# Kernel optimization log

Measured on AMD Instinct MI355X. Metric: run time of the kernel, lower is better.

## Reference

```python
import jax, jax.numpy as jnp
import numpy as np

H1, H2, H3 = 128, 64, 32   # hidden sizes from source constants
NT = 2                      # n_targets (P_I_meas, Q_I_meas)
NF = 16                     # n_features
B, T, S = 4096, 200, 20     # batch, history length, OUTPUT_STEPS


def setup_inputs() -> dict:
    key = jax.random.key(0)
    ks = jax.random.split(key, 16)
    s1 = 1.0 / np.sqrt(H1)  # pytorch LSTM init scale
    s2 = 1.0 / np.sqrt(H2)
    s3 = 1.0 / np.sqrt(H3)
    f32 = jnp.float32
    return {
        "x_history": jax.random.normal(ks[0], (B, T, NF), dtype=f32),
        "x_future_refs": jax.random.normal(ks[1], (B, S, NF - NT), dtype=f32),
        "Wih1": jax.random.normal(ks[2], (4 * H1, NF), dtype=f32) * s1,
        "Whh1": jax.random.normal(ks[3], (4 * H1, H1), dtype=f32) * s1,
        "bih1": jax.random.normal(ks[4], (4 * H1,), dtype=f32) * s1,
        "bhh1": jax.random.normal(ks[5], (4 * H1,), dtype=f32) * s1,
        "Wih2": jax.random.normal(ks[6], (4 * H2, H1), dtype=f32) * s2,
        "Whh2": jax.random.normal(ks[7], (4 * H2, H2), dtype=f32) * s2,
        "bih2": jax.random.normal(ks[8], (4 * H2,), dtype=f32) * s2,
        "bhh2": jax.random.normal(ks[9], (4 * H2,), dtype=f32) * s2,
        "Wd": jax.random.normal(ks[10], (H3, H2), dtype=f32) * s2,
        "bd": jax.random.normal(ks[11], (H3,), dtype=f32) * s2,
        "Wf": jax.random.normal(ks[12], (NT, H3), dtype=f32) * s3,
        "bf": jax.random.normal(ks[13], (NT,), dtype=f32) * s3,
        "out_bias": jnp.zeros((NT,), dtype=f32),
    }


def lstm_cell(x, h, c, Wih, Whh, bih, bhh):
    # PyTorch gate order: i, f, g, o
    g = x @ Wih.T + h @ Whh.T + (bih + bhh)
    i, f, gg, o = jnp.split(g, 4, axis=-1)
    c_new = jax.nn.sigmoid(f) * c + jax.nn.sigmoid(i) * jnp.tanh(gg)
    h_new = jax.nn.sigmoid(o) * jnp.tanh(c_new)
    return h_new, c_new


def reference(x_history, x_future_refs, Wih1, Whh1, bih1, bhh1,
              Wih2, Whh2, bih2, bhh2, Wd, bd, Wf, bf, out_bias):
    b = x_history.shape[0]
    dt = x_history.dtype
    h1 = jnp.zeros((b, H1), dt); c1 = jnp.zeros((b, H1), dt)
    h2 = jnp.zeros((b, H2), dt); c2 = jnp.zeros((b, H2), dt)

    # --- encode history: stacked 2-layer LSTM over T steps ---
    def enc_step(carry, xt):
        h1, c1, h2, c2 = carry
        h1, c1 = lstm_cell(xt, h1, c1, Wih1, Whh1, bih1, bhh1)
        h2, c2 = lstm_cell(h1, h2, c2, Wih2, Whh2, bih2, bhh2)
        return (h1, c1, h2, c2), None

    (h1, c1, h2, c2), _ = jax.lax.scan(
        enc_step, (h1, c1, h2, c2), jnp.swapaxes(x_history, 0, 1))

    # last history targets: x_history[:, -1, n_non_targets:]
    cur = x_history[:, -1, NF - NT:]

    def dec_step(carry, ref):
        h1, c1, h2, c2, cur = carry
        xin = jnp.concatenate([ref, cur], axis=1)  # [B, NF]
        h1, c1 = lstm_cell(xin, h1, c1, Wih1, Whh1, bih1, bhh1)
        h2, c2 = lstm_cell(h1, h2, c2, Wih2, Whh2, bih2, bhh2)
        d = jax.nn.relu(h2 @ Wd.T + bd)
        pred = d @ Wf.T + bf + out_bias
        return (h1, c1, h2, c2, pred), pred

    _, preds = jax.lax.scan(
        dec_step, (h1, c1, h2, c2, cur), jnp.swapaxes(x_future_refs, 0, 1))
    return jnp.swapaxes(preds, 0, 1)  # [B, S, NT]
```

## Files before the change

kernel.cpp:

```cpp
#include <hip/hip_runtime.h>

typedef unsigned short u16;
typedef unsigned int u32;

using short8 = __attribute__((ext_vector_type(8))) short;
using f32x4  = __attribute__((ext_vector_type(4))) float;
using float4v = __attribute__((ext_vector_type(4))) float;

#define LOG2E 1.44269504088896340736f

#define X1S 136
#define H2S 72
#define DBS 40
#define XCS 328

__device__ __forceinline__ u16 f2bf(float f) {
  u32 u = __float_as_uint(f);
  return (u16)((u + 0x7FFFu + ((u >> 16) & 1u)) >> 16);
}
__device__ __forceinline__ float sigm(float x) {
  return __builtin_amdgcn_rcpf(1.0f + __builtin_amdgcn_exp2f(-LOG2E * x));
}
__device__ __forceinline__ float tanh_(float x) {
  return 1.0f - 2.0f * __builtin_amdgcn_rcpf(1.0f + __builtin_amdgcn_exp2f(2.0f * LOG2E * x));
}
__device__ __forceinline__ f32x4 mfma_(short8 a, short8 b, f32x4 c) {
  return __builtin_amdgcn_mfma_f32_16x16x32_bf16(a, b, c, 0, 0, 0);
}

__global__ __launch_bounds__(512, 1) void spc_lstm(
    const float* __restrict__ xh,   const float* __restrict__ xfr,
    const float* __restrict__ Wih1, const float* __restrict__ Whh1,
    const float* __restrict__ bih1, const float* __restrict__ bhh1,
    const float* __restrict__ Wih2, const float* __restrict__ Whh2,
    const float* __restrict__ bih2, const float* __restrict__ bhh2,
    const float* __restrict__ Wd,   const float* __restrict__ bd,
    const float* __restrict__ Wf,   const float* __restrict__ bfv,
    const float* __restrict__ ob,   float* __restrict__ out)
{
  __shared__ __align__(16) u16 X1[2][16 * X1S];
  __shared__ __align__(16) u16 H2B[2][16 * H2S];
  __shared__ __align__(16) u16 DB[16 * DBS];
  __shared__ __align__(16) u16 W1xF[32 * 512];
  __shared__ __align__(16) u16 W2F[64 * 512];
  __shared__ __align__(16) u16 WdF[4 * 512];
  __shared__ __align__(16) u16 WfF[512];
  __shared__ __align__(16) u16 XCH[2][16 * XCS];

  const int tid = threadIdx.x;
  const int wv  = tid >> 6;
  const int l   = tid & 63;
  const int c   = l & 15;
  const int q   = l >> 4;
  const int bb  = blockIdx.x << 4;
  const bool isA = (wv < 4);

  short8 w1h[4][4];
  short8 w2h[4][2];
  float  b1r[4];
  float  b2r[4] = {0.f, 0.f, 0.f, 0.f};

  for (int i = tid; i < 2 * 16 * X1S; i += 512) ((u16*)X1)[i] = 0;
  for (int i = tid; i < 2 * 16 * H2S; i += 512) ((u16*)H2B)[i] = 0;
  for (int i = tid; i < 16 * DBS; i += 512) DB[i] = 0;
  for (int i = tid; i < 2 * 16 * XCS; i += 512) ((u16*)XCH)[i] = 0;
  __syncthreads();

  for (int i = tid; i < 64 * 512; i += 512) {
    const int rid = i >> 9, e = i & 511, k = e >> 4, n = e & 15;
    const int ww = rid >> 4, ty = (rid >> 2) & 3, kc = rid & 3;
    const int g = ty * 64 + ww * 16 + n;
    W2F[rid * 512 + ((k >> 3) * 16 + n) * 8 + (k & 7)] = f2bf(Wih2[g * 128 + kc * 32 + k]);
  }
  for (int i = tid; i < 32 * 512; i += 512) {
    const int T = i >> 9, e = i & 511, k = e >> 4, n = e & 15;
    const int ty = T >> 3, uv = T & 7;
    const int g = ty * 128 + uv * 16 + n;
    W1xF[T * 512 + ((k >> 3) * 16 + n) * 8 + (k & 7)] =
        (k < 16) ? f2bf(Wih1[g * 16 + k]) : (u16)0;
  }
  for (int i = tid; i < 4 * 512; i += 512) {
    const int tix = i >> 9, e = i & 511, k = e >> 4, n = e & 15;
    const int ww = tix >> 1, kc2 = tix & 1;
    WdF[tix * 512 + ((k >> 3) * 16 + n) * 8 + (k & 7)] =
        f2bf(Wd[(ww * 16 + n) * 64 + kc2 * 32 + k]);
  }
  {
    const int k = tid >> 4, n = tid & 15;
    if (tid < 512)
      WfF[((k >> 3) * 16 + n) * 8 + (k & 7)] = (n < 2) ? f2bf(Wf[n * 32 + k]) : (u16)0;
  }

  if (!isA) {
    const int i0 = tid - 256;
    #pragma unroll
    for (int p = 0; p < 2; p++) {
      const int idx = i0 + p * 256;
      const int r = idx >> 5, rem = idx & 31, st = rem >> 2, hf = rem & 3;
      const float4v v = *(const float4v*)&xh[(bb + r) * 3200 + st * 16 + hf * 4];
      u16* d = &XCH[0][r * XCS + st * 40 + hf * 4];
      d[0] = f2bf(v[0]); d[1] = f2bf(v[1]); d[2] = f2bf(v[2]); d[3] = f2bf(v[3]);
    }
  }

  #pragma unroll
  for (int ty = 0; ty < 4; ty++) {
    const int g = ty * 128 + wv * 16 + c;
    b1r[ty] = bih1[g] + bhh1[g];
    #pragma unroll
    for (int kc = 0; kc < 4; kc++) {
      short8 v;
      #pragma unroll
      for (int j = 0; j < 8; j++)
        v[j] = (short)f2bf(Whh1[g * 128 + kc * 32 + q * 8 + j]);
      w1h[ty][kc] = v;
    }
  }
  if (isA) {
    #pragma unroll
    for (int ty = 0; ty < 4; ty++) {
      const int g2 = ty * 64 + wv * 16 + c;
      b2r[ty] = bih2[g2] + bhh2[g2];
      #pragma unroll
      for (int kc = 0; kc < 2; kc++) {
        short8 v;
        #pragma unroll
        for (int j = 0; j < 8; j++)
          v[j] = (short)f2bf(Whh2[g2 * 64 + kc * 32 + q * 8 + j]);
        w2h[ty][kc] = v;
      }
    }
  }
  const float bdr = (wv == 4 || wv == 5) ? bd[(wv - 4) * 16 + c] : 0.f;
  const float bfr = (wv == 4 && c < 2) ? (bfv[c] + ob[c]) : 0.f;

  f32x4 c1 = (f32x4){0,0,0,0};
  f32x4 c2 = (f32x4){0,0,0,0};
  __syncthreads();

  for (int t = 0; t <= 220; t++) {
    u16* Xc    = X1[t & 1];
    u16* Xn    = X1[(t + 1) & 1];
    u16* Hprev = H2B[t & 1];
    u16* Hdst  = H2B[(t + 1) & 1];
    const bool dec  = (t >= 201);
    const bool doL1 = (t <= 219);
    const bool doL2 = isA && (t >= 1);

    if (!isA && (t & 7) == 0) {
      const int cm = (t >> 3) + 1;
      if (cm <= 27) {
        u16* dst = XCH[cm & 1];
        const int t0 = cm << 3;
        if (cm <= 24) {
          const int i0 = tid - 256;
          #pragma unroll
          for (int p = 0; p < 2; p++) {
            const int idx = i0 + p * 256;
            const int r = idx >> 5, rem = idx & 31, st = rem >> 2, hf = rem & 3;
            const float4v v = *(const float4v*)&xh[(bb + r) * 3200 + (t0 + st) * 16 + hf * 4];
            u16* d = &dst[r * XCS + st * 40 + hf * 4];
            d[0] = f2bf(v[0]); d[1] = f2bf(v[1]); d[2] = f2bf(v[2]); d[3] = f2bf(v[3]);
          }
        } else {
          for (int e = tid - 256; e < 16 * 8 * 14; e += 256) {
            const int r = e / 112, rem2 = e % 112, st = rem2 / 14, f = rem2 % 14;
            const int s8 = t0 + st;
            if (s8 < 220)
              dst[r * XCS + st * 40 + f] = f2bf(xfr[(bb + r) * 280 + (s8 - 200) * 14 + f]);
          }
          if (cm == 25) {
            const int e = tid - 256;
            if (e < 32) {
              const int r = e >> 1, f = 14 + (e & 1);
              dst[r * XCS + f] = f2bf(xh[(bb + r) * 3200 + 199 * 16 + f]);
            }
          }
        }
      }
    }

    if (doL2) {
      f32x4 acc2[4];
      #pragma unroll
      for (int ty = 0; ty < 4; ty++)
        acc2[ty] = (f32x4){b2r[ty], b2r[ty], b2r[ty], b2r[ty]};
      #pragma unroll
      for (int kc = 0; kc < 4; kc++) {
        const short8 fhi = *(const short8*)&Xc[c * X1S + kc * 32 + q * 8];
        #pragma unroll
        for (int ty = 0; ty < 4; ty++) {
          const short8 wf_ = *(const short8*)&W2F[(wv * 16 + ty * 4 + kc) * 512 + l * 8];
          acc2[ty] = mfma_(fhi, wf_, acc2[ty]);
        }
      }
      #pragma unroll
      for (int kc = 0; kc < 2; kc++) {
        const short8 hhi = *(const short8*)&Hprev[c * H2S + kc * 32 + q * 8];
        #pragma unroll
        for (int ty = 0; ty < 4; ty++)
          acc2[ty] = mfma_(hhi, w2h[ty][kc], acc2[ty]);
      }
      const int u = wv * 16 + c;
      #pragma unroll
      for (int r = 0; r < 4; r++) {
        float ig = sigm(acc2[0][r]);
        float fg = sigm(acc2[1][r]);
        float gg = tanh_(acc2[2][r]);
        float og = sigm(acc2[3][r]);
        float cn = fg * c2[r] + ig * gg;
        float hn = og * tanh_(cn);
        c2[r] = cn;
        Hdst[(q * 4 + r) * H2S + u] = f2bf(hn);
      }
    }

    if (dec) {
      __syncthreads();
      if (wv == 4 || wv == 5) {
        const int ww = wv - 4;
        f32x4 accd = (f32x4){bdr, bdr, bdr, bdr};
        #pragma unroll
        for (int kc = 0; kc < 2; kc++) {
          const short8 ad  = *(const short8*)&Hdst[c * H2S + kc * 32 + q * 8];
          const short8 wdk = *(const short8*)&WdF[(ww * 2 + kc) * 512 + l * 8];
          accd = mfma_(ad, wdk, accd);
        }
        #pragma unroll
        for (int r = 0; r < 4; r++)
          DB[(q * 4 + r) * DBS + ww * 16 + c] = f2bf(fmaxf(accd[r], 0.f));
      }
      __syncthreads();
      if (wv == 4) {
        const short8 ap  = *(const short8*)&DB[c * DBS + q * 8];
        const short8 wfv = *(const short8*)&WfF[l * 8];
        f32x4 accp = (f32x4){bfr, bfr, bfr, bfr};
        accp = mfma_(ap, wfv, accp);
        if (c < 2) {
          u16* slot = &XCH[(t >> 3) & 1][0];
          #pragma unroll
          for (int r = 0; r < 4; r++) {
            const int b = q * 4 + r;
            out[(bb + b) * 40 + (t - 201) * 2 + c] = accp[r];
            slot[b * XCS + (t & 7) * 40 + 14 + c] = f2bf(accp[r]);
          }
        }
      }
      __syncthreads();
    }

    if (doL1) {
      f32x4 acc1[4];
      #pragma unroll
      for (int ty = 0; ty < 4; ty++)
        acc1[ty] = (f32x4){b1r[ty], b1r[ty], b1r[ty], b1r[ty]};
      #pragma unroll
      for (int kc = 0; kc < 4; kc++) {
        const short8 ahi = *(const short8*)&Xc[c * X1S + kc * 32 + q * 8];
        #pragma unroll
        for (int ty = 0; ty < 4; ty++)
          acc1[ty] = mfma_(ahi, w1h[ty][kc], acc1[ty]);
      }
      {
        const short8 ax =
            *(const short8*)&XCH[(t >> 3) & 1][c * XCS + (t & 7) * 40 + q * 8];
        #pragma unroll
        for (int ty = 0; ty < 4; ty++) {
          const short8 wxv = *(const short8*)&W1xF[(ty * 8 + wv) * 512 + l * 8];
          acc1[ty] = mfma_(ax, wxv, acc1[ty]);
        }
      }
      const int u = wv * 16 + c;
      #pragma unroll
      for (int r = 0; r < 4; r++) {
        float ig = sigm(acc1[0][r]);
        float fg = sigm(acc1[1][r]);
        float gg = tanh_(acc1[2][r]);
        float og = sigm(acc1[3][r]);
        float cn = fg * c1[r] + ig * gg;
        float hn = og * tanh_(cn);
        c1[r] = cn;
        Xn[(q * 4 + r) * X1S + u] = f2bf(hn);
      }
    }
    __syncthreads();
  }
}

extern "C" void kernel_launch(void* const* d_in, const int* in_sizes, int n_in,
                              void* d_out, int out_size, void* d_ws, size_t ws_size,
                              hipStream_t stream) {
  (void)in_sizes; (void)n_in; (void)out_size; (void)d_ws; (void)ws_size;
  spc_lstm<<<dim3(256), dim3(512), 0, stream>>>(
      (const float*)d_in[0],  (const float*)d_in[1],
      (const float*)d_in[2],  (const float*)d_in[3],
      (const float*)d_in[4],  (const float*)d_in[5],
      (const float*)d_in[6],  (const float*)d_in[7],
      (const float*)d_in[8],  (const float*)d_in[9],
      (const float*)d_in[10], (const float*)d_in[11],
      (const float*)d_in[12], (const float*)d_in[13],
      (const float*)d_in[14], (float*)d_out);
}
```

Baseline: 459.9 us.

## Split layer-1 and layer-2 LSTM work onto separate waves with 768 threads

Expands the block from 8 to 12 waves so that 8 waves compute only layer 1 and 4 dedicated waves compute layer 2, instead of waves 0-3 doing both layers serially. Layer-2 waves also take over input prefetching and the decoder head. This is meant to shorten the per-timestep critical path by running both layers concurrently. The cost is more threads per block, sharing of register files and SIMDs, and a larger barrier group.

```diff
diff --git a/kernel.cpp b/kernel.cpp
--- a/kernel.cpp
+++ b/kernel.cpp
@@ -28,7 +28,7 @@
   return __builtin_amdgcn_mfma_f32_16x16x32_bf16(a, b, c, 0, 0, 0);
 }
 
-__global__ __launch_bounds__(512, 1) void spc_lstm(
+__global__ __launch_bounds__(768, 1) void spc_lstm(
     const float* __restrict__ xh,   const float* __restrict__ xfr,
     const float* __restrict__ Wih1, const float* __restrict__ Whh1,
     const float* __restrict__ bih1, const float* __restrict__ bhh1,
@@ -53,33 +53,32 @@
   const int c   = l & 15;
   const int q   = l >> 4;
   const int bb  = blockIdx.x << 4;
-  const bool isA = (wv < 4);
-
-  short8 w1h[4][4];
-  short8 w2h[4][2];
-  float  b1r[4];
-  float  b2r[4] = {0.f, 0.f, 0.f, 0.f};
-
-  for (int i = tid; i < 2 * 16 * X1S; i += 512) ((u16*)X1)[i] = 0;
-  for (int i = tid; i < 2 * 16 * H2S; i += 512) ((u16*)H2B)[i] = 0;
-  for (int i = tid; i < 16 * DBS; i += 512) DB[i] = 0;
-  for (int i = tid; i < 2 * 16 * XCS; i += 512) ((u16*)XCH)[i] = 0;
+  const bool isL1 = (wv < 8);
+  const int w2  = wv - 8;
+
+  short8 wreg[4][4];
+  float  br[4];
+
+  for (int i = tid; i < 2 * 16 * X1S; i += 768) ((u16*)X1)[i] = 0;
+  for (int i = tid; i < 2 * 16 * H2S; i += 768) ((u16*)H2B)[i] = 0;
+  for (int i = tid; i < 16 * DBS; i += 768) DB[i] = 0;
+  for (int i = tid; i < 2 * 16 * XCS; i += 768) ((u16*)XCH)[i] = 0;
   __syncthreads();
 
-  for (int i = tid; i < 64 * 512; i += 512) {
+  for (int i = tid; i < 64 * 512; i += 768) {
     const int rid = i >> 9, e = i & 511, k = e >> 4, n = e & 15;
     const int ww = rid >> 4, ty = (rid >> 2) & 3, kc = rid & 3;
     const int g = ty * 64 + ww * 16 + n;
     W2F[rid * 512 + ((k >> 3) * 16 + n) * 8 + (k & 7)] = f2bf(Wih2[g * 128 + kc * 32 + k]);
   }
-  for (int i = tid; i < 32 * 512; i += 512) {
+  for (int i = tid; i < 32 * 512; i += 768) {
     const int T = i >> 9, e = i & 511, k = e >> 4, n = e & 15;
     const int ty = T >> 3, uv = T & 7;
     const int g = ty * 128 + uv * 16 + n;
     W1xF[T * 512 + ((k >> 3) * 16 + n) * 8 + (k & 7)] =
         (k < 16) ? f2bf(Wih1[g * 16 + k]) : (u16)0;
   }
-  for (int i = tid; i < 4 * 512; i += 512) {
+  for (int i = tid; i < 4 * 512; i += 768) {
     const int tix = i >> 9, e = i & 511, k = e >> 4, n = e & 15;
     const int ww = tix >> 1, kc2 = tix & 1;
     WdF[tix * 512 + ((k >> 3) * 16 + n) * 8 + (k & 7)] =
@@ -91,8 +90,8 @@
       WfF[((k >> 3) * 16 + n) * 8 + (k & 7)] = (n < 2) ? f2bf(Wf[n * 32 + k]) : (u16)0;
   }
 
-  if (!isA) {
-    const int i0 = tid - 256;
+  if (!isL1) {
+    const int i0 = tid - 512;
     #pragma unroll
     for (int p = 0; p < 2; p++) {
       const int idx = i0 + p * 256;
@@ -103,39 +102,41 @@
     }
   }
 
-  #pragma unroll
-  for (int ty = 0; ty < 4; ty++) {
-    const int g = ty * 128 + wv * 16 + c;
-    b1r[ty] = bih1[g] + bhh1[g];
-    #pragma unroll
-    for (int kc = 0; kc < 4; kc++) {
-      short8 v;
-      #pragma unroll
-      for (int j = 0; j < 8; j++)
-        v[j] = (short)f2bf(Whh1[g * 128 + kc * 32 + q * 8 + j]);
-      w1h[ty][kc] = v;
-    }
-  }
-  if (isA) {
+  if (isL1) {
     #pragma unroll
     for (int ty = 0; ty < 4; ty++) {
-      const int g2 = ty * 64 + wv * 16 + c;
-      b2r[ty] = bih2[g2] + bhh2[g2];
+      const int g = ty * 128 + wv * 16 + c;
+      br[ty] = bih1[g] + bhh1[g];
+      #pragma unroll
+      for (int kc = 0; kc < 4; kc++) {
+        short8 v;
+        #pragma unroll
+        for (int j = 0; j < 8; j++)
+          v[j] = (short)f2bf(Whh1[g * 128 + kc * 32 + q * 8 + j]);
+        wreg[ty][kc] = v;
+      }
+    }
+  } else {
+    #pragma unroll
+    for (int ty = 0; ty < 4; ty++) {
+      const int g2 = ty * 64 + w2 * 16 + c;
+      br[ty] = bih2[g2] + bhh2[g2];
       #pragma unroll
       for (int kc = 0; kc < 2; kc++) {
         short8 v;
         #pragma unroll
         for (int j = 0; j < 8; j++)
           v[j] = (short)f2bf(Whh2[g2 * 64 + kc * 32 + q * 8 + j]);
-        w2h[ty][kc] = v;
-      }
-    }
-  }
-  const float bdr = (wv == 4 || wv == 5) ? bd[(wv - 4) * 16 + c] : 0.f;
-  const float bfr = (wv == 4 && c < 2) ? (bfv[c] + ob[c]) : 0.f;
-
-  f32x4 c1 = (f32x4){0,0,0,0};
-  f32x4 c2 = (f32x4){0,0,0,0};
+        wreg[ty][kc] = v;
+      }
+      wreg[ty][2] = (short8){0,0,0,0,0,0,0,0};
+      wreg[ty][3] = (short8){0,0,0,0,0,0,0,0};
+    }
+  }
+  const float bdr = (wv == 8 || wv == 9) ? bd[(wv - 8) * 16 + c] : 0.f;
+  const float bfr = (wv == 8 && c < 2) ? (bfv[c] + ob[c]) : 0.f;
+
+  f32x4 cst = (f32x4){0,0,0,0};
   __syncthreads();
 
   for (int t = 0; t <= 220; t++) {
@@ -144,16 +145,16 @@
     u16* Hprev = H2B[t & 1];
     u16* Hdst  = H2B[(t + 1) & 1];
     const bool dec  = (t >= 201);
-    const bool doL1 = (t <= 219);
-    const bool doL2 = isA && (t >= 1);
-
-    if (!isA && (t & 7) == 0) {
+    const bool doL1 = isL1 && (t <= 219);
+    const bool doL2 = !isL1 && (t >= 1);
+
+    if (!isL1 && (t & 7) == 0) {
       const int cm = (t >> 3) + 1;
       if (cm <= 27) {
         u16* dst = XCH[cm & 1];
         const int t0 = cm << 3;
         if (cm <= 24) {
-          const int i0 = tid - 256;
+          const int i0 = tid - 512;
           #pragma unroll
           for (int p = 0; p < 2; p++) {
             const int idx = i0 + p * 256;
@@ -163,14 +164,14 @@
             d[0] = f2bf(v[0]); d[1] = f2bf(v[1]); d[2] = f2bf(v[2]); d[3] = f2bf(v[3]);
           }
         } else {
-          for (int e = tid - 256; e < 16 * 8 * 14; e += 256) {
+          for (int e = tid - 512; e < 16 * 8 * 14; e += 256) {
             const int r = e / 112, rem2 = e % 112, st = rem2 / 14, f = rem2 % 14;
             const int s8 = t0 + st;
             if (s8 < 220)
               dst[r * XCS + st * 40 + f] = f2bf(xfr[(bb + r) * 280 + (s8 - 200) * 14 + f]);
           }
           if (cm == 25) {
-            const int e = tid - 256;
+            const int e = tid - 512;
             if (e < 32) {
               const int r = e >> 1, f = 14 + (e & 1);
               dst[r * XCS + f] = f2bf(xh[(bb + r) * 3200 + 199 * 16 + f]);
@@ -184,13 +185,13 @@
       f32x4 acc2[4];
       #pragma unroll
       for (int ty = 0; ty < 4; ty++)
-        acc2[ty] = (f32x4){b2r[ty], b2r[ty], b2r[ty], b2r[ty]};
+        acc2[ty] = (f32x4){br[ty], br[ty], br[ty], br[ty]};
       #pragma unroll
       for (int kc = 0; kc < 4; kc++) {
         const short8 fhi = *(const short8*)&Xc[c * X1S + kc * 32 + q * 8];
         #pragma unroll
         for (int ty = 0; ty < 4; ty++) {
-          const short8 wf_ = *(const short8*)&W2F[(wv * 16 + ty * 4 + kc) * 512 + l * 8];
+          const short8 wf_ = *(const short8*)&W2F[(w2 * 16 + ty * 4 + kc) * 512 + l * 8];
           acc2[ty] = mfma_(fhi, wf_, acc2[ty]);
         }
       }
@@ -199,26 +200,26 @@
         const short8 hhi = *(const short8*)&Hprev[c * H2S + kc * 32 + q * 8];
         #pragma unroll
         for (int ty = 0; ty < 4; ty++)
-          acc2[ty] = mfma_(hhi, w2h[ty][kc], acc2[ty]);
-      }
-      const int u = wv * 16 + c;
+          acc2[ty] = mfma_(hhi, wreg[ty][kc], acc2[ty]);
+      }
+      const int u = w2 * 16 + c;
       #pragma unroll
       for (int r = 0; r < 4; r++) {
         float ig = sigm(acc2[0][r]);
         float fg = sigm(acc2[1][r]);
         float gg = tanh_(acc2[2][r]);
         float og = sigm(acc2[3][r]);
-        float cn = fg * c2[r] + ig * gg;
+        float cn = fg * cst[r] + ig * gg;
         float hn = og * tanh_(cn);
-        c2[r] = cn;
+        cst[r] = cn;
         Hdst[(q * 4 + r) * H2S + u] = f2bf(hn);
       }
     }
 
     if (dec) {
       __syncthreads();
-      if (wv == 4 || wv == 5) {
-        const int ww = wv - 4;
+      if (wv == 8 || wv == 9) {
+        const int ww = wv - 8;
         f32x4 accd = (f32x4){bdr, bdr, bdr, bdr};
         #pragma unroll
         for (int kc = 0; kc < 2; kc++) {
@@ -231,7 +232,7 @@
           DB[(q * 4 + r) * DBS + ww * 16 + c] = f2bf(fmaxf(accd[r], 0.f));
       }
       __syncthreads();
-      if (wv == 4) {
+      if (wv == 8) {
         const short8 ap  = *(const short8*)&DB[c * DBS + q * 8];
         const short8 wfv = *(const short8*)&WfF[l * 8];
         f32x4 accp = (f32x4){bfr, bfr, bfr, bfr};
@@ -253,13 +254,13 @@
       f32x4 acc1[4];
       #pragma unroll
       for (int ty = 0; ty < 4; ty++)
-        acc1[ty] = (f32x4){b1r[ty], b1r[ty], b1r[ty], b1r[ty]};
+        acc1[ty] = (f32x4){br[ty], br[ty], br[ty], br[ty]};
       #pragma unroll
       for (int kc = 0; kc < 4; kc++) {
         const short8 ahi = *(const short8*)&Xc[c * X1S + kc * 32 + q * 8];
         #pragma unroll
         for (int ty = 0; ty < 4; ty++)
-          acc1[ty] = mfma_(ahi, w1h[ty][kc], acc1[ty]);
+          acc1[ty] = mfma_(ahi, wreg[ty][kc], acc1[ty]);
       }
       {
         const short8 ax =
@@ -277,9 +278,9 @@
         float fg = sigm(acc1[1][r]);
         float gg = tanh_(acc1[2][r]);
         float og = sigm(acc1[3][r]);
-        float cn = fg * c1[r] + ig * gg;
+        float cn = fg * cst[r] + ig * gg;
         float hn = og * tanh_(cn);
-        c1[r] = cn;
+        cst[r] = cn;
         Xn[(q * 4 + r) * X1S + u] = f2bf(hn);
       }
     }
@@ -291,7 +292,7 @@
                               void* d_out, int out_size, void* d_ws, size_t ws_size,
                               hipStream_t stream) {
   (void)in_sizes; (void)n_in; (void)out_size; (void)d_ws; (void)ws_size;
-  spc_lstm<<<dim3(256), dim3(512), 0, stream>>>(
+  spc_lstm<<<dim3(256), dim3(768), 0, stream>>>(
       (const float*)d_in[0],  (const float*)d_in[1],
       (const float*)d_in[2],  (const float*)d_in[3],
       (const float*)d_in[4],  (const float*)d_in[5],
```

Result: no change. 465.3 us (+1.2%).
